# Kernel tuning notes

Hardware: AMD Instinct MI355X
Metric: run time of the kernel (lower is better)

Reference implementation:

```python
import jax, jax.numpy as jnp
import numpy as np


def setup_inputs() -> dict:
    key = jax.random.key(0)
    features = jax.random.normal(key, (8192, 512), dtype=jnp.float32)
    return {"features": features}


def reference(features):
    # Pairwise L2 distance via the GEMM trick (avoids the N x N x D broadcast
    # intermediate the original torch code materializes):
    #   ||a - b||^2 = ||a||^2 + ||b||^2 - 2 a.b
    sq_norms = jnp.sum(features * features, axis=-1)            # [N]
    gram = features @ features.T                                # [N, N]
    sq_dist = sq_norms[:, None] + sq_norms[None, :] - 2.0 * gram
    sq_dist = jnp.maximum(sq_dist, 0.0)                         # clamp fp noise
    return -jnp.sqrt(sq_dist)                                   # [N, N]
```

## Files before the change

### kernel.cpp

```cpp
#include <hip/hip_runtime.h>
#include <hip/hip_bf16.h>
#include <math.h>

#define N_ROWS 8192
#define DIM    512

typedef __bf16 bf16x8 __attribute__((ext_vector_type(8)));
typedef float  floatx4 __attribute__((ext_vector_type(4)));

__device__ __forceinline__ unsigned short f2bf_rne(float x) {
    union { float f; unsigned u; } v; v.f = x;
    unsigned r = v.u + 0x7FFFu + ((v.u >> 16) & 1u);
    return (unsigned short)(r >> 16);
}

__device__ __forceinline__ void async_cp16(const void* g, void* l) {
    __builtin_amdgcn_global_load_lds(
        (const __attribute__((address_space(1))) unsigned int*)g,
        (__attribute__((address_space(3))) unsigned int*)l,
        16, 0, 0);
}

__global__ __launch_bounds__(256) void fs_norm_convert(
    const float* __restrict__ F, unsigned short* __restrict__ Fb,
    float* __restrict__ sn) {
    const int wave = threadIdx.x >> 6;
    const int lane = threadIdx.x & 63;
    const int row  = blockIdx.x * 4 + wave;

    const float4* src = reinterpret_cast<const float4*>(F + (size_t)row * DIM) + lane * 2;
    float4 x0 = src[0];
    float4 x1 = src[1];

    float ss = x0.x*x0.x + x0.y*x0.y + x0.z*x0.z + x0.w*x0.w
             + x1.x*x1.x + x1.y*x1.y + x1.z*x1.z + x1.w*x1.w;

    uint4 p;
    p.x = (unsigned)f2bf_rne(x0.x) | ((unsigned)f2bf_rne(x0.y) << 16);
    p.y = (unsigned)f2bf_rne(x0.z) | ((unsigned)f2bf_rne(x0.w) << 16);
    p.z = (unsigned)f2bf_rne(x1.x) | ((unsigned)f2bf_rne(x1.y) << 16);
    p.w = (unsigned)f2bf_rne(x1.z) | ((unsigned)f2bf_rne(x1.w) << 16);
    reinterpret_cast<uint4*>(Fb + (size_t)row * DIM)[lane] = p;

    #pragma unroll
    for (int off = 32; off > 0; off >>= 1) ss += __shfl_down(ss, off);
    if (lane == 0) sn[row] = ss;
}

__global__ __launch_bounds__(256) void fs_gemm(
    const unsigned short* __restrict__ Fb, const float* __restrict__ sn,
    float* __restrict__ out) {
    __shared__ unsigned short As[128 * 32];
    __shared__ unsigned short Bs[128 * 32];

    const int tid  = threadIdx.x;
    const int lane = tid & 63;
    const int wave = tid >> 6;
    const int wr   = wave >> 1;
    const int wc   = wave & 1;
    const int quad = lane >> 4;
    const int l16  = lane & 15;

    const int bRow = blockIdx.y * 128;
    const int bCol = blockIdx.x * 128;

    floatx4 acc[4][4];
    #pragma unroll
    for (int i = 0; i < 4; ++i)
        #pragma unroll
        for (int j = 0; j < 4; ++j)
            acc[i][j] = floatx4{0.f, 0.f, 0.f, 0.f};

    const int sRow = tid >> 2;
    const int sCol = (tid & 3) * 8;
    const unsigned short* gA = Fb + (size_t)(bRow + sRow) * DIM + sCol;
    const unsigned short* gB = Fb + (size_t)(bCol + sRow) * DIM + sCol;
    const size_t half = (size_t)64 * DIM;

    unsigned short* ldsA = As + tid * 8;
    unsigned short* ldsB = Bs + tid * 8;

    for (int k0 = 0; k0 < DIM; k0 += 32) {
        async_cp16(gA,        ldsA);
        async_cp16(gA + half, ldsA + 2048);
        async_cp16(gB,        ldsB);
        async_cp16(gB + half, ldsB + 2048);
        gA += 32; gB += 32;
        __syncthreads();

        bf16x8 af[4], bf[4];
        #pragma unroll
        for (int t = 0; t < 4; ++t) {
            af[t] = *reinterpret_cast<const bf16x8*>(
                As + ((wr * 64 + t * 16 + l16) * 32 + quad * 8));
            bf[t] = *reinterpret_cast<const bf16x8*>(
                Bs + ((wc * 64 + t * 16 + l16) * 32 + quad * 8));
        }
        #pragma unroll
        for (int i = 0; i < 4; ++i)
            #pragma unroll
            for (int j = 0; j < 4; ++j)
                acc[i][j] = __builtin_amdgcn_mfma_f32_16x16x32_bf16(
                    af[i], bf[j], acc[i][j], 0, 0, 0);
        __syncthreads();
    }

    const int row0 = bRow + wr * 64;
    const int col0 = bCol + wc * 64;
    float snc[4];
    #pragma unroll
    for (int j = 0; j < 4; ++j) snc[j] = sn[col0 + j * 16 + l16];

    #pragma unroll
    for (int i = 0; i < 4; ++i) {
        #pragma unroll
        for (int r = 0; r < 4; ++r) {
            const int row = row0 + i * 16 + quad * 4 + r;
            const float snr = sn[row];
            float* orow = out + (size_t)row * N_ROWS;
            #pragma unroll
            for (int j = 0; j < 4; ++j) {
                const int col = col0 + j * 16 + l16;
                float v = snr + snc[j] - 2.0f * acc[i][j][r];
                v = fmaxf(v, 0.0f);
                orow[col] = (row == col) ? 0.0f : -sqrtf(v);
            }
        }
    }
}

extern "C" void kernel_launch(void* const* d_in, const int* in_sizes, int n_in,
                              void* d_out, int out_size, void* d_ws, size_t ws_size,
                              hipStream_t stream) {
    const float* F = (const float*)d_in[0];
    float* out = (float*)d_out;

    unsigned short* Fb = (unsigned short*)d_ws;
    float* sn = (float*)((char*)d_ws + (size_t)N_ROWS * DIM * 2);

    fs_norm_convert<<<N_ROWS / 4, 256, 0, stream>>>(F, Fb, sn);

    dim3 grid(N_ROWS / 128, N_ROWS / 128);
    fs_gemm<<<grid, 256, 0, stream>>>(Fb, sn, out);
}
```

Baseline: 350.5 us.

## Exploit Gram symmetry: compute lower-triangular tiles and mirror-write transposes

Launches only the lower-triangular 128x128 tiles of the distance matrix, found from a linear block index by triangular-number inversion. Each off-diagonal tile also writes its transpose with float4 stores. This roughly halves the MFMA work and operand loads while keeping the full output write volume. In exchange the transposed stores are strided across rows, and the grid is half as large, which may hurt load balance.

```diff
diff --git a/kernel.cpp b/kernel.cpp
--- a/kernel.cpp
+++ b/kernel.cpp
@@ -47,7 +47,7 @@
     if (lane == 0) sn[row] = ss;
 }
 
-__global__ __launch_bounds__(256) void fs_gemm(
+__global__ __launch_bounds__(256) void fs_gemm_sym(
     const unsigned short* __restrict__ Fb, const float* __restrict__ sn,
     float* __restrict__ out) {
     __shared__ unsigned short As[128 * 32];
@@ -61,8 +61,14 @@
     const int quad = lane >> 4;
     const int l16  = lane & 15;
 
-    const int bRow = blockIdx.y * 128;
-    const int bCol = blockIdx.x * 128;
+    const int b = blockIdx.x;
+    int br = (int)((sqrtf(8.0f * (float)b + 1.0f) - 1.0f) * 0.5f);
+    while ((br + 1) * (br + 2) / 2 <= b) ++br;
+    while (br * (br + 1) / 2 > b) --br;
+    const int bc = b - br * (br + 1) / 2;
+
+    const int bRow = br * 128;
+    const int bCol = bc * 128;
 
     floatx4 acc[4][4];
     #pragma unroll
@@ -107,12 +113,14 @@
 
     const int row0 = bRow + wr * 64;
     const int col0 = bCol + wc * 64;
+    const bool mirror = (br != bc);
     float snc[4];
     #pragma unroll
     for (int j = 0; j < 4; ++j) snc[j] = sn[col0 + j * 16 + l16];
 
     #pragma unroll
     for (int i = 0; i < 4; ++i) {
+        float vv[4][4];
         #pragma unroll
         for (int r = 0; r < 4; ++r) {
             const int row = row0 + i * 16 + quad * 4 + r;
@@ -123,7 +131,18 @@
                 const int col = col0 + j * 16 + l16;
                 float v = snr + snc[j] - 2.0f * acc[i][j][r];
                 v = fmaxf(v, 0.0f);
-                orow[col] = (row == col) ? 0.0f : -sqrtf(v);
+                v = (row == col) ? 0.0f : -sqrtf(v);
+                vv[j][r] = v;
+                orow[col] = v;
+            }
+        }
+        if (mirror) {
+            const int rbase = row0 + i * 16 + quad * 4;
+            #pragma unroll
+            for (int j = 0; j < 4; ++j) {
+                const int col = col0 + j * 16 + l16;
+                float4 m = make_float4(vv[j][0], vv[j][1], vv[j][2], vv[j][3]);
+                *reinterpret_cast<float4*>(out + (size_t)col * N_ROWS + rbase) = m;
             }
         }
     }
@@ -140,6 +159,6 @@
 
     fs_norm_convert<<<N_ROWS / 4, 256, 0, stream>>>(F, Fb, sn);
 
-    dim3 grid(N_ROWS / 128, N_ROWS / 128);
-    fs_gemm<<<grid, 256, 0, stream>>>(Fb, sn, out);
+    const int nblk = (N_ROWS / 128) * (N_ROWS / 128 + 1) / 2;
+    fs_gemm_sym<<<nblk, 256, 0, stream>>>(Fb, sn, out);
 }
```

New measurement: 362.9 us. +3.5%, slower.
